# Kernel tuning notes

Hardware: AMD Instinct MI355X
Metric: run time of the kernel (lower is better)

The kernel has to match this reference:

```python
import jax, jax.numpy as jnp
import numpy as np

OFFSET_BINS = np.array([0.0, 0.00794435329, 0.0158887021, 0.0238330509, 0.0317773996,
                        0.0397217484, 0.0476660972, 0.0556104459, 0.0635547947,
                        0.0714991435, 0.08], dtype=np.float32)
BIN_WEIGHTS = jnp.array([0.16652107, 0.21488856, 0.37031708, 0.55618503, 0.75124664,
                         0.93943357, 1.07824539, 1.19423112, 1.55731375, 2.34173634],
                        dtype=jnp.float32)
RADIUS = 0.005
FAR = 1.0e5
EPS = 1e-7


def setup_inputs():
    key = jax.random.key(0)
    ks = jax.random.split(key, 10)
    B, N, M, C = 4, 2048, 4096, 5
    return {
        'pred_grasps': jax.random.normal(ks[0], (B, N, 4, 4), jnp.float32) * 0.1,
        'pred_scores': jax.random.uniform(ks[1], (B, N, 1), jnp.float32, 1e-4, 1.0 - 1e-4),
        'pred_points': jax.random.uniform(ks[2], (B, N, 3), jnp.float32) * 0.1,
        'grasp_width_head': jax.random.normal(ks[3], (B, 10, N), jnp.float32),
        'pos_contact_points': jax.random.uniform(ks[4], (B, M, 3), jnp.float32) * 0.1,
        'pos_contact_width': jax.random.uniform(ks[5], (B, M), jnp.float32) * 0.08,
        'pos_contact_rot': jax.random.normal(ks[6], (B, M, 3, 3), jnp.float32),
        'pos_contact_trans': jax.random.uniform(ks[7], (B, M, 3), jnp.float32) * 0.1,
        'gripper_control_points': jax.random.normal(ks[8], (1, C, 3), jnp.float32) * 0.05,
        'gripper_control_points_sym': jax.random.normal(ks[9], (1, C, 3), jnp.float32) * 0.05,
        'epoch': 0,
    }


def _gather(a, idx):
    # a: (B, M, ...), idx: (B, N) -> (B, N, ...)
    return jax.vmap(lambda x, j: x[j])(a, idx)


def _pairwise_sq(a, b):
    # a: (B,N,3), b: (B,M,3) -> (B,N,M) squared distances via norm expansion
    an = jnp.sum(a * a, -1)
    bn = jnp.sum(b * b, -1)
    cross = jnp.einsum('bnd,bmd->bnm', a, b)
    return jnp.maximum(an[:, :, None] + bn[:, None, :] - 2.0 * cross, 0.0)


def _pair_min_cp(P, G):
    # P,G: (B,N,C,3) control point sets -> (B,N) min_j sum_{c,d}(P_i - G_j)^2
    pn = jnp.sum(P * P, axis=(2, 3))
    gn = jnp.sum(G * G, axis=(2, 3))
    cross = jnp.einsum('bicd,bjcd->bij', P, G)  # (B,N,N)
    sq = pn[:, :, None] + gn[:, None, :] - 2.0 * cross
    return jnp.min(sq, axis=2)


def _forward(pred_grasps, pred_scores, pred_points, grasp_width_head,
             pos_contact_points, pos_contact_width, pos_contact_rot,
             pos_contact_trans, gripper_control_points, gripper_control_points_sym):
    B, N, _ = pred_points.shape
    # ---- labels: nearest GT contact per predicted point (nsample=1) ----
    d2 = _pairwise_sq(pred_points, pos_contact_points)          # (B,N,M)
    idx = jnp.argmin(d2, axis=2)                                 # (B,N)
    min_d2 = jnp.take_along_axis(d2, idx[:, :, None], axis=2)[..., 0]
    width_label = _gather(pos_contact_width, idx)[..., None]     # (B,N,1)
    success = (min_d2 < RADIUS ** 2).astype(jnp.float32)[..., None]  # (B,N,1)
    rot_label = _gather(pos_contact_rot, idx)                    # (B,N,3,3)
    trans_label = _gather(pos_contact_trans, idx)                # (B,N,3)

    pos_in_view = jnp.clip(jnp.sum(success, axis=1), 1.0, None)  # (B,1)

    # ---- binary score loss with balanced pos/neg sampling ----
    p = jnp.clip(pred_scores, EPS, 1.0 - EPS)
    bce = -(success * jnp.log(p) + (1.0 - success) * jnp.log(1.0 - p))[..., 0]  # (B,N)
    pos = success[..., 0]
    neg = 1.0 - pos
    n_pos = jnp.sum(pos, axis=1)                                 # (B,)
    r = jax.random.uniform(jax.random.key(42), (B, N))
    pri = jnp.where(neg > 0.5, r, jnp.inf)
    rank = jnp.argsort(jnp.argsort(pri, axis=1), axis=1)         # random ranks over negatives
    k = jnp.where(n_pos > 0, n_pos, 2.0)
    sel_neg = ((rank < k[:, None]) & (neg > 0.5)).astype(jnp.float32)
    sel = pos + sel_neg
    bin_ce_loss = jnp.mean(jnp.sum(bce * sel, axis=1) / jnp.maximum(jnp.sum(sel, axis=1), 1.0))

    # ---- width loss: multihot bins + weighted BCE-with-logits ----
    lo = jnp.asarray(OFFSET_BINS[:-1])
    hi = jnp.asarray(OFFSET_BINS[1:])
    multihot = ((width_label >= lo) & (width_label < hi)).astype(jnp.float32)  # (B,N,10)
    x = jnp.transpose(grasp_width_head, (0, 2, 1))               # (B,N,10)
    bcew = jnp.maximum(x, 0.0) - x * multihot + jnp.log1p(jnp.exp(-jnp.abs(x)))
    wl = jnp.mean(BIN_WEIGHTS[None, None, :] * bcew, axis=2)     # (B,N)
    width_loss = jnp.mean(jnp.sum(wl * pos, axis=1, keepdims=True) / pos_in_view)

    # ---- ADD-S loss ----
    mask = success > 0.5                                          # (B,N,1)
    rot_l = jnp.where(mask[..., None], rot_label, FAR)
    trans_l = jnp.where(mask, trans_label, FAR)
    cp = gripper_control_points[0]                                # (C,3)
    cps = gripper_control_points_sym[0]
    pred_rot = pred_grasps[:, :, :3, :3]
    pred_trans = pred_grasps[:, :, :3, 3]
    P = jnp.einsum('bnij,cj->bnci', pred_rot, cp) + pred_trans[:, :, None, :]
    G = jnp.einsum('bnij,cj->bnci', rot_l, cp) + trans_l[:, :, None, :]
    Gs = jnp.einsum('bnij,cj->bnci', rot_l, cps) + trans_l[:, :, None, :]
    m = jnp.minimum(_pair_min_cp(P, G), _pair_min_cp(P, Gs))     # (B,N)
    min_adds = pos * jnp.sqrt(jnp.maximum(m, 0.0) + 1e-12)
    adds = jnp.sum(pred_scores[..., 0] * min_adds, axis=1) / pos_in_view[:, 0]
    adds_loss = jnp.mean(adds)

    total_loss = bin_ce_loss + width_loss + 3.0 * adds_loss
    return total_loss, bin_ce_loss, width_loss, adds_loss


def reference(pred_grasps, pred_scores, pred_points, grasp_width_head,
              pos_contact_points, pos_contact_width, pos_contact_rot,
              pos_contact_trans, gripper_control_points, gripper_control_points_sym, epoch):
    return _forward(pred_grasps, pred_scores, pred_points, grasp_width_head,
                    pos_contact_points, pos_contact_width, pos_contact_rot,
                    pos_contact_trans, gripper_control_points, gripper_control_points_sym)
```

## Files before the change

kernel.cpp:

```cpp
#include <hip/hip_runtime.h>
#include <math.h>

#define B_ 4
#define N_ 2048
#define M_ 4096

#define ADDS_BLOCKS (B_ * (N_ / 16) * 2)
#define RANK_BLOCKS (B_ * (N_ / 16))

__constant__ float c_LO[10] = {0.0f, 0.00794435329f, 0.0158887021f, 0.0238330509f,
                               0.0317773996f, 0.0397217484f, 0.0476660972f,
                               0.0556104459f, 0.0635547947f, 0.0714991435f};
__constant__ float c_HI[10] = {0.00794435329f, 0.0158887021f, 0.0238330509f,
                               0.0317773996f, 0.0397217484f, 0.0476660972f,
                               0.0556104459f, 0.0635547947f, 0.0714991435f, 0.08f};
__constant__ float c_BW[10] = {0.16652107f, 0.21488856f, 0.37031708f, 0.55618503f,
                               0.75124664f, 0.93943357f, 1.07824539f, 1.19423112f,
                               1.55731375f, 2.34173634f};

#define R2_ 2.5e-05f
#define FAR_ 100000.0f
#define EPS_ 1e-07f

__device__ inline unsigned rotl32(unsigned x, int d) { return (x << d) | (x >> (32 - d)); }

__device__ inline void threefry2x32_42(unsigned x0, unsigned x1, unsigned& o0, unsigned& o1) {
    const unsigned k0 = 0u, k1 = 42u;
    const unsigned k2 = k0 ^ k1 ^ 0x1BD11BDAu;
    const unsigned ks[3] = {k0, k1, k2};
    const int rot[2][4] = {{13, 15, 26, 6}, {17, 29, 16, 24}};
    unsigned v0 = x0 + k0;
    unsigned v1 = x1 + k1;
#pragma unroll
    for (int i = 0; i < 5; ++i) {
        const int* r = rot[i & 1];
#pragma unroll
        for (int j = 0; j < 4; ++j) {
            v0 += v1;
            v1 = rotl32(v1, r[j]);
            v1 ^= v0;
        }
        v0 += ks[(i + 1) % 3];
        v1 += ks[(i + 2) % 3] + (unsigned)(i + 1);
    }
    o0 = v0; o1 = v1;
}

__device__ inline float bits_to_uniform(unsigned bits) {
    float f = __uint_as_float((bits >> 9) | 0x3f800000u) - 1.0f;
    return fmaxf(0.0f, f);
}

__device__ inline float jax_uniform_r(int flat) {
    unsigned o0, o1;
    if (flat < 4096) {
        threefry2x32_42((unsigned)flat, (unsigned)(flat + 4096), o0, o1);
        return bits_to_uniform(o0);
    } else {
        threefry2x32_42((unsigned)(flat - 4096), (unsigned)flat, o0, o1);
        return bits_to_uniform(o1);
    }
}

__global__ __launch_bounds__(256, 4) void nn_prep_kernel(
        const float* __restrict__ ppts, const float* __restrict__ pcp,
        const float* __restrict__ pred_grasps,
        const float* __restrict__ rot, const float* __restrict__ trans,
        const float* __restrict__ cp, const float* __restrict__ cps,
        int* __restrict__ idx_out, float* __restrict__ d2_out,
        float* __restrict__ Pout, float* __restrict__ Gt,
        int* __restrict__ counters) {
    if (blockIdx.x == 0 && threadIdx.x == 0) { counters[0] = 0; counters[1] = 0; }
    int blk = blockIdx.x;
    int b = blk / (N_ / 8);
    int tile = blk % (N_ / 8);
    int tid = threadIdx.x;
    int ig = tid & 1;
    int part = tid >> 1;
    int i0 = tile * 8 + ig * 4;

    float ax[4], ay[4], az[4], an[4];
#pragma unroll
    for (int ii = 0; ii < 4; ++ii) {
        const float* pp = ppts + ((size_t)b * N_ + i0 + ii) * 3;
        ax[ii] = pp[0]; ay[ii] = pp[1]; az[ii] = pp[2];
        an[ii] = ax[ii] * ax[ii] + ay[ii] * ay[ii] + az[ii] * az[ii];
    }

    const float4* pb4 = reinterpret_cast<const float4*>(pcp + (size_t)b * M_ * 3);
    float best[4] = {INFINITY, INFINITY, INFINITY, INFINITY};
    int bidx[4] = {0, 0, 0, 0};
    for (int g = 0; g < 8; ++g) {
        int grp = g * 128 + part;
        float4 q0 = pb4[grp * 3 + 0];
        float4 q1 = pb4[grp * 3 + 1];
        float4 q2 = pb4[grp * 3 + 2];
        float px[4] = {q0.x, q0.w, q1.z, q2.y};
        float py[4] = {q0.y, q1.x, q1.w, q2.z};
        float pz[4] = {q0.z, q1.y, q2.x, q2.w};
#pragma unroll
        for (int k = 0; k < 4; ++k) {
            float bn = px[k] * px[k] + py[k] * py[k] + pz[k] * pz[k];
            int j = grp * 4 + k;
#pragma unroll
            for (int ii = 0; ii < 4; ++ii) {
                float cross = ax[ii] * px[k] + ay[ii] * py[k] + az[ii] * pz[k];
                float d = an[ii] + bn - 2.0f * cross;
                d = fmaxf(d, 0.0f);
                if (d < best[ii]) { best[ii] = d; bidx[ii] = j; }
            }
        }
    }

    __shared__ float sd[8][128];
    __shared__ int si[8][128];
    __shared__ int win_bi[8];
    __shared__ float win_bb[8];
    __shared__ float rt[8][12];
#pragma unroll
    for (int ii = 0; ii < 4; ++ii) {
        sd[ig * 4 + ii][part] = best[ii];
        si[ig * 4 + ii][part] = bidx[ii];
    }
    __syncthreads();

    {
        int i2 = tid >> 5, r = tid & 31;
        float bb = sd[i2][r * 4];
        int bi = si[i2][r * 4];
#pragma unroll
        for (int p = 1; p < 4; ++p) {
            float dv = sd[i2][r * 4 + p];
            int iv = si[i2][r * 4 + p];
            if (dv < bb || (dv == bb && iv < bi)) { bb = dv; bi = iv; }
        }
        __syncthreads();
        sd[i2][r] = bb; si[i2][r] = bi;
    }
    __syncthreads();
    if (tid < 64) {
        int i2 = tid >> 3, r = tid & 7;
        float bb = sd[i2][r * 4];
        int bi = si[i2][r * 4];
#pragma unroll
        for (int p = 1; p < 4; ++p) {
            float dv = sd[i2][r * 4 + p];
            int iv = si[i2][r * 4 + p];
            if (dv < bb || (dv == bb && iv < bi)) { bb = dv; bi = iv; }
        }
        __syncthreads();
        sd[i2][r] = bb; si[i2][r] = bi;
    } else {
        __syncthreads();
    }
    __syncthreads();
    if (tid < 8) {
        float bb = sd[tid][0];
        int bi = si[tid][0];
#pragma unroll
        for (int p = 1; p < 8; ++p) {
            float dv = sd[tid][p];
            int iv = si[tid][p];
            if (dv < bb || (dv == bb && iv < bi)) { bb = dv; bi = iv; }
        }
        int n = tile * 8 + tid;
        idx_out[b * N_ + n] = bi;
        d2_out[b * N_ + n] = bb;
        win_bi[tid] = bi;
        win_bb[tid] = bb;
    }
    __syncthreads();

    if (tid < 96) {
        int n2 = tid / 12, c = tid % 12;
        int bi2 = win_bi[n2];
        bool succ2 = win_bb[n2] < R2_;
        float v;
        if (succ2) {
            v = (c < 9) ? rot[((size_t)b * M_ + bi2) * 9 + c]
                        : trans[((size_t)b * M_ + bi2) * 3 + (c - 9)];
        } else {
            v = FAR_;
        }
        rt[n2][c] = v;
    }
    __syncthreads();

    if (tid < 8) {
        int n = tile * 8 + tid;
        size_t i = (size_t)b * N_ + n;
        const float* g = pred_grasps + i * 16;
        float R[3][3] = {{g[0], g[1], g[2]}, {g[4], g[5], g[6]}, {g[8], g[9], g[10]}};
        float t[3] = {g[3], g[7], g[11]};

        float* P = Pout + i * 16;
        float pn = 0.0f;
#pragma unroll
        for (int c = 0; c < 5; ++c) {
            float cx = cp[c * 3], cy = cp[c * 3 + 1], cz = cp[c * 3 + 2];
#pragma unroll
            for (int kk = 0; kk < 3; ++kk) {
                float v = R[kk][0] * cx + R[kk][1] * cy + R[kk][2] * cz + t[kk];
                P[c * 3 + kk] = v;
                pn += v * v;
            }
        }
        P[15] = pn;

        float RL[3][3] = {{rt[tid][0], rt[tid][1], rt[tid][2]},
                          {rt[tid][3], rt[tid][4], rt[tid][5]},
                          {rt[tid][6], rt[tid][7], rt[tid][8]}};
        float TL[3] = {rt[tid][9], rt[tid][10], rt[tid][11]};

        float* gtb = Gt + ((size_t)b * 8 * N_ + n) * 4;
        float gn = 0.0f, gsn = 0.0f;
#pragma unroll
        for (int c = 0; c < 5; ++c) {
            float cx = cp[c * 3], cy = cp[c * 3 + 1], cz = cp[c * 3 + 2];
#pragma unroll
            for (int kk = 0; kk < 3; ++kk) {
                int comp = c * 3 + kk;
                float v = RL[kk][0] * cx + RL[kk][1] * cy + RL[kk][2] * cz + TL[kk];
                gtb[(size_t)(comp >> 2) * (N_ * 4) + (comp & 3)] = v;
                gn += v * v;
            }
        }
        gtb[(size_t)(15 >> 2) * (N_ * 4) + (15 & 3)] = gn;
#pragma unroll
        for (int c = 0; c < 5; ++c) {
            float cx = cps[c * 3], cy = cps[c * 3 + 1], cz = cps[c * 3 + 2];
#pragma unroll
            for (int kk = 0; kk < 3; ++kk) {
                int comp = 16 + c * 3 + kk;
                float v = RL[kk][0] * cx + RL[kk][1] * cy + RL[kk][2] * cz + TL[kk];
                gtb[(size_t)(comp >> 2) * (N_ * 4) + (comp & 3)] = v;
                gsn += v * v;
            }
        }
        gtb[(size_t)(31 >> 2) * (N_ * 4) + (31 & 3)] = gsn;
    }
}

__global__ __launch_bounds__(256, 4) void work_kernel(
        const float* __restrict__ Parr, const float4* __restrict__ Gt4,
        float* __restrict__ mOut2,
        const float* __restrict__ d2w, float* __restrict__ selws) {
    __shared__ __align__(16) char smem[9600];
    int bid = blockIdx.x;
    int tid = threadIdx.x;

    if (bid < ADDS_BLOCKS) {
        int b = bid / (2 * (N_ / 16));
        int rem = bid % (2 * (N_ / 16));
        int tile = rem >> 1;
        int jh = rem & 1;
        int w = tid >> 6;
        int lane = tid & 63;
        int i0 = tile * 16 + w * 4;

        const float4* P4 = reinterpret_cast<const float4*>(Parr) +
                           ((size_t)b * N_ + i0) * 4;
        float Pv[4][16];
#pragma unroll
        for (int h = 0; h < 4; ++h)
#pragma unroll
            for (int q = 0; q < 4; ++q) {
                float4 v = P4[h * 4 + q];
                Pv[h][q * 4 + 0] = v.x; Pv[h][q * 4 + 1] = v.y;
                Pv[h][q * 4 + 2] = v.z; Pv[h][q * 4 + 3] = v.w;
            }

        const float4* gq = Gt4 + (size_t)b * 8 * N_;
        float best[4] = {INFINITY, INFINITY, INFINITY, INFINITY};
        int jb0 = jh * (N_ / 128);
        for (int jb = jb0; jb < jb0 + (N_ / 128); ++jb) {
            int j = jb * 64 + lane;
            float g[16];
            {
                float4 h0 = gq[(size_t)0 * N_ + j];
                float4 h1 = gq[(size_t)1 * N_ + j];
                float4 h2 = gq[(size_t)2 * N_ + j];
                float4 h3 = gq[(size_t)3 * N_ + j];
                g[0] = h0.x; g[1] = h0.y; g[2] = h0.z; g[3] = h0.w;
                g[4] = h1.x; g[5] = h1.y; g[6] = h1.z; g[7] = h1.w;
                g[8] = h2.x; g[9] = h2.y; g[10] = h2.z; g[11] = h2.w;
                g[12] = h3.x; g[13] = h3.y; g[14] = h3.z; g[15] = h3.w;
            }
            float s1[4];
            {
                float d[4] = {0.0f, 0.0f, 0.0f, 0.0f};
#pragma unroll
                for (int q = 0; q < 15; ++q)
#pragma unroll
                    for (int ii = 0; ii < 4; ++ii) d[ii] += Pv[ii][q] * g[q];
#pragma unroll
                for (int ii = 0; ii < 4; ++ii) s1[ii] = Pv[ii][15] + g[15] - 2.0f * d[ii];
            }
            {
                float4 h0 = gq[(size_t)4 * N_ + j];
                float4 h1 = gq[(size_t)5 * N_ + j];
                float4 h2 = gq[(size_t)6 * N_ + j];
                float4 h3 = gq[(size_t)7 * N_ + j];
                g[0] = h0.x; g[1] = h0.y; g[2] = h0.z; g[3] = h0.w;
                g[4] = h1.x; g[5] = h1.y; g[6] = h1.z; g[7] = h1.w;
                g[8] = h2.x; g[9] = h2.y; g[10] = h2.z; g[11] = h2.w;
                g[12] = h3.x; g[13] = h3.y; g[14] = h3.z; g[15] = h3.w;
            }
            {
                float d[4] = {0.0f, 0.0f, 0.0f, 0.0f};
#pragma unroll
                for (int q = 0; q < 15; ++q)
#pragma unroll
                    for (int ii = 0; ii < 4; ++ii) d[ii] += Pv[ii][q] * g[q];
#pragma unroll
                for (int ii = 0; ii < 4; ++ii) {
                    float s2 = Pv[ii][15] + g[15] - 2.0f * d[ii];
                    best[ii] = fminf(best[ii], fminf(s1[ii], s2));
                }
            }
        }
#pragma unroll
        for (int m = 32; m > 0; m >>= 1) {
#pragma unroll
            for (int ii = 0; ii < 4; ++ii)
                best[ii] = fminf(best[ii], __shfl_xor(best[ii], m));
        }
        if (lane == 0) {
#pragma unroll
            for (int ii = 0; ii < 4; ++ii)
                mOut2[(size_t)(b * N_ + i0 + ii) * 2 + jh] = best[ii];
        }
    } else {
        int rid = bid - ADDS_BLOCKS;
        int b = rid / (N_ / 16);
        int tile = rid % (N_ / 16);
        int n_local = tid & 15;
        int part = tid >> 4;

        float* pri = (float*)smem;
        int* cnt_sh = (int*)(smem + 8192);
        __shared__ int s_npos;
        if (tid == 0) s_npos = 0;
        __syncthreads();

        int lp = 0;
        for (int q = tid; q < N_; q += 256) {
            bool pos = d2w[b * N_ + q] < R2_;
            pri[q] = pos ? INFINITY : jax_uniform_r(b * N_ + q);
            if (pos) lp++;
        }
        atomicAdd(&s_npos, lp);
        __syncthreads();

        int n = tile * 16 + n_local;
        float ra = pri[n];

        int cnt = 0;
        const float4* p4 = reinterpret_cast<const float4*>(pri);
        for (int o = 0; o < 8; ++o) {
            float4 v[4];
#pragma unroll
            for (int k = 0; k < 4; ++k) v[k] = p4[part + (o * 4 + k) * 16];
#pragma unroll
            for (int k = 0; k < 4; ++k) {
                int qb = (part + (o * 4 + k) * 16) * 4;
                cnt += ((v[k].x < ra) || (v[k].x == ra && (qb + 0) < n)) ? 1 : 0;
                cnt += ((v[k].y < ra) || (v[k].y == ra && (qb + 1) < n)) ? 1 : 0;
                cnt += ((v[k].z < ra) || (v[k].z == ra && (qb + 2) < n)) ? 1 : 0;
                cnt += ((v[k].w < ra) || (v[k].w == ra && (qb + 3) < n)) ? 1 : 0;
            }
        }
        cnt_sh[part * 17 + n_local] = cnt;
        __syncthreads();

        if (tid < 16) {
            int tot = 0;
#pragma unroll
            for (int p = 0; p < 16; ++p) tot += cnt_sh[p * 17 + tid];
            int npos = s_npos;
            int kk = (npos > 0) ? npos : 2;
            int n2 = tile * 16 + tid;
            float r2 = pri[n2];
            selws[b * N_ + n2] = (r2 == INFINITY) ? 1.0f : ((tot < kk) ? 1.0f : 0.0f);
        }
    }
}

__global__ __launch_bounds__(256) void finalize_kernel(
        const float* __restrict__ scores, const float* __restrict__ gwh,
        const float* __restrict__ pcw, const int* __restrict__ idxw,
        const float* __restrict__ d2w, const float* __restrict__ mw2,
        const float* __restrict__ selws,
        float* __restrict__ partials, int* __restrict__ counters,
        float* __restrict__ out) {
    int fid = blockIdx.x;
    int b = fid >> 3;
    int part = fid & 7;
    int tid = threadIdx.x;
    int n = part * 256 + tid;
    __shared__ float wsum[4][5];

    float sc = scores[b * N_ + n];
    float pcl = fminf(fmaxf(sc, EPS_), 0.9999999f);
    bool pos = d2w[b * N_ + n] < R2_;
    float s = pos ? 1.0f : 0.0f;
    float bce = -(s * logf(pcl) + (1.0f - s) * logf(1.0f - pcl));
    float selv = selws[b * N_ + n];
    float sum_sel = selv;
    float sum_bce = bce * selv;
    float sum_pos = s;
    float sum_wl = 0.0f, sum_adds = 0.0f;
    if (pos) {
        int jx = idxw[b * N_ + n];
        float w = pcw[b * M_ + jx];
        float acc = 0.0f;
#pragma unroll
        for (int jb = 0; jb < 10; ++jb) {
            float x = gwh[((size_t)b * 10 + jb) * N_ + n];
            float mh = (w >= c_LO[jb] && w < c_HI[jb]) ? 1.0f : 0.0f;
            float bw = fmaxf(x, 0.0f) - x * mh + log1pf(expf(-fabsf(x)));
            acc += c_BW[jb] * bw;
        }
        sum_wl = acc * 0.1f;
        float mv = fminf(mw2[(size_t)(b * N_ + n) * 2 + 0],
                         mw2[(size_t)(b * N_ + n) * 2 + 1]);
        sum_adds = sc * sqrtf(fmaxf(mv, 0.0f) + 1e-12f);
    }

    float v0 = sum_sel, v1 = sum_bce, v2 = sum_wl, v3 = sum_adds, v4 = sum_pos;
#pragma unroll
    for (int off = 32; off > 0; off >>= 1) {
        v0 += __shfl_down(v0, off);
        v1 += __shfl_down(v1, off);
        v2 += __shfl_down(v2, off);
        v3 += __shfl_down(v3, off);
        v4 += __shfl_down(v4, off);
    }
    int wv = tid >> 6, lane = tid & 63;
    if (lane == 0) {
        wsum[wv][0] = v0; wsum[wv][1] = v1; wsum[wv][2] = v2;
        wsum[wv][3] = v3; wsum[wv][4] = v4;
    }
    __syncthreads();
    if (tid == 0) {
        float t0 = 0, t1 = 0, t2 = 0, t3 = 0, t4 = 0;
#pragma unroll
        for (int w = 0; w < 4; ++w) {
            t0 += wsum[w][0]; t1 += wsum[w][1]; t2 += wsum[w][2];
            t3 += wsum[w][3]; t4 += wsum[w][4];
        }
        float* pp = partials + (size_t)fid * 5;
        pp[0] = t0; pp[1] = t1; pp[2] = t2; pp[3] = t3; pp[4] = t4;
        __threadfence();
        int old = atomicAdd(&counters[1], 1);
        if (old == 32 - 1) {
            __threadfence();
            float bin = 0, wid = 0, ad = 0;
#pragma unroll
            for (int b2 = 0; b2 < B_; ++b2) {
                float u0 = 0, u1 = 0, u2 = 0, u3 = 0, u4 = 0;
#pragma unroll
                for (int p2 = 0; p2 < 8; ++p2) {
                    const float* q = partials + (size_t)(b2 * 8 + p2) * 5;
                    u0 += q[0]; u1 += q[1]; u2 += q[2]; u3 += q[3]; u4 += q[4];
                }
                float piv = fmaxf(u4, 1.0f);
                bin += u1 / fmaxf(u0, 1.0f);
                wid += u2 / piv;
                ad  += u3 / piv;
            }
            bin *= 0.25f; wid *= 0.25f; ad *= 0.25f;
            out[0] = bin + wid + 3.0f * ad;
            out[1] = bin;
            out[2] = wid;
            out[3] = ad;
        }
    }
}

extern "C" void kernel_launch(void* const* d_in, const int* in_sizes, int n_in,
                              void* d_out, int out_size, void* d_ws, size_t ws_size,
                              hipStream_t stream) {
    const float* pred_grasps = (const float*)d_in[0];
    const float* pred_scores = (const float*)d_in[1];
    const float* pred_points = (const float*)d_in[2];
    const float* gwh         = (const float*)d_in[3];
    const float* pcp         = (const float*)d_in[4];
    const float* pcw         = (const float*)d_in[5];
    const float* pcr         = (const float*)d_in[6];
    const float* pct         = (const float*)d_in[7];
    const float* cp          = (const float*)d_in[8];
    const float* cps         = (const float*)d_in[9];
    (void)in_sizes; (void)n_in; (void)out_size; (void)ws_size;

    float* ws = (float*)d_ws;
    int*   idxw  = (int*)ws;
    float* d2w   = ws + 8192;
    float* Pw    = ws + 16384;
    float* Gt    = Pw + 131072;
    float* mw2   = Gt + 262144;
    float* selws = mw2 + 16384;
    float* parts = selws + 8192;
    int*   ctrs  = (int*)(parts + 160);
    float* outp  = (float*)d_out;

    hipLaunchKernelGGL(nn_prep_kernel, dim3(B_ * (N_ / 8)), dim3(256), 0, stream,
                       pred_points, pcp, pred_grasps, pcr, pct, cp, cps,
                       idxw, d2w, Pw, Gt, ctrs);
    hipLaunchKernelGGL(work_kernel, dim3(ADDS_BLOCKS + RANK_BLOCKS), dim3(256), 0, stream,
                       Pw, (const float4*)Gt, mw2, d2w, selws);
    hipLaunchKernelGGL(finalize_kernel, dim3(B_ * 8), dim3(256), 0, stream,
                       pred_scores, gwh, pcw, idxw, d2w, mw2, selws, parts, ctrs, outp);
}
```

Before: 132.2 us.

## Fuse finalize into work kernel using atomic completion counter and spin-wait

Merges the finalize kernel into the work kernel as its last 32 blocks. Each producer block bumps a release atomic counter when done, and the finalize blocks spin on it with s_sleep before reducing. This removes one kernel launch and the launch gap between the two stages. The spin-wait relies on the producer blocks being scheduled before or alongside the waiting blocks, and waiting blocks hold CU slots while they spin.

```diff
diff --git a/kernel.cpp b/kernel.cpp
--- a/kernel.cpp
+++ b/kernel.cpp
@@ -7,6 +7,8 @@
 
 #define ADDS_BLOCKS (B_ * (N_ / 16) * 2)
 #define RANK_BLOCKS (B_ * (N_ / 16))
+#define PROD_BLOCKS (ADDS_BLOCKS + RANK_BLOCKS)
+#define FIN_BLOCKS (B_ * 8)
 
 __constant__ float c_LO[10] = {0.0f, 0.00794435329f, 0.0158887021f, 0.0238330509f,
                                0.0317773996f, 0.0397217484f, 0.0476660972f,
@@ -241,10 +243,14 @@
     }
 }
 
-__global__ __launch_bounds__(256, 4) void work_kernel(
+__global__ __launch_bounds__(256, 4) void mega_kernel(
         const float* __restrict__ Parr, const float4* __restrict__ Gt4,
         float* __restrict__ mOut2,
-        const float* __restrict__ d2w, float* __restrict__ selws) {
+        const float* __restrict__ d2w, float* __restrict__ selws,
+        const float* __restrict__ scores, const float* __restrict__ gwh,
+        const float* __restrict__ pcw, const int* __restrict__ idxw,
+        float* __restrict__ partials, int* __restrict__ counters,
+        float* __restrict__ out) {
     __shared__ __align__(16) char smem[9600];
     int bid = blockIdx.x;
     int tid = threadIdx.x;
@@ -330,7 +336,13 @@
             for (int ii = 0; ii < 4; ++ii)
                 mOut2[(size_t)(b * N_ + i0 + ii) * 2 + jh] = best[ii];
         }
-    } else {
+        __syncthreads();
+        if (tid == 0) {
+            __threadfence();
+            __hip_atomic_fetch_add(&counters[0], 1, __ATOMIC_RELEASE,
+                                   __HIP_MEMORY_SCOPE_AGENT);
+        }
+    } else if (bid < PROD_BLOCKS) {
         int rid = bid - ADDS_BLOCKS;
         int b = rid / (N_ / 16);
         int tile = rid % (N_ / 16);
@@ -383,97 +395,104 @@
             float r2 = pri[n2];
             selws[b * N_ + n2] = (r2 == INFINITY) ? 1.0f : ((tot < kk) ? 1.0f : 0.0f);
         }
-    }
-}
-
-__global__ __launch_bounds__(256) void finalize_kernel(
-        const float* __restrict__ scores, const float* __restrict__ gwh,
-        const float* __restrict__ pcw, const int* __restrict__ idxw,
-        const float* __restrict__ d2w, const float* __restrict__ mw2,
-        const float* __restrict__ selws,
-        float* __restrict__ partials, int* __restrict__ counters,
-        float* __restrict__ out) {
-    int fid = blockIdx.x;
-    int b = fid >> 3;
-    int part = fid & 7;
-    int tid = threadIdx.x;
-    int n = part * 256 + tid;
-    __shared__ float wsum[4][5];
-
-    float sc = scores[b * N_ + n];
-    float pcl = fminf(fmaxf(sc, EPS_), 0.9999999f);
-    bool pos = d2w[b * N_ + n] < R2_;
-    float s = pos ? 1.0f : 0.0f;
-    float bce = -(s * logf(pcl) + (1.0f - s) * logf(1.0f - pcl));
-    float selv = selws[b * N_ + n];
-    float sum_sel = selv;
-    float sum_bce = bce * selv;
-    float sum_pos = s;
-    float sum_wl = 0.0f, sum_adds = 0.0f;
-    if (pos) {
-        int jx = idxw[b * N_ + n];
-        float w = pcw[b * M_ + jx];
-        float acc = 0.0f;
-#pragma unroll
-        for (int jb = 0; jb < 10; ++jb) {
-            float x = gwh[((size_t)b * 10 + jb) * N_ + n];
-            float mh = (w >= c_LO[jb] && w < c_HI[jb]) ? 1.0f : 0.0f;
-            float bw = fmaxf(x, 0.0f) - x * mh + log1pf(expf(-fabsf(x)));
-            acc += c_BW[jb] * bw;
-        }
-        sum_wl = acc * 0.1f;
-        float mv = fminf(mw2[(size_t)(b * N_ + n) * 2 + 0],
-                         mw2[(size_t)(b * N_ + n) * 2 + 1]);
-        sum_adds = sc * sqrtf(fmaxf(mv, 0.0f) + 1e-12f);
-    }
-
-    float v0 = sum_sel, v1 = sum_bce, v2 = sum_wl, v3 = sum_adds, v4 = sum_pos;
-#pragma unroll
-    for (int off = 32; off > 0; off >>= 1) {
-        v0 += __shfl_down(v0, off);
-        v1 += __shfl_down(v1, off);
-        v2 += __shfl_down(v2, off);
-        v3 += __shfl_down(v3, off);
-        v4 += __shfl_down(v4, off);
-    }
-    int wv = tid >> 6, lane = tid & 63;
-    if (lane == 0) {
-        wsum[wv][0] = v0; wsum[wv][1] = v1; wsum[wv][2] = v2;
-        wsum[wv][3] = v3; wsum[wv][4] = v4;
-    }
-    __syncthreads();
-    if (tid == 0) {
-        float t0 = 0, t1 = 0, t2 = 0, t3 = 0, t4 = 0;
-#pragma unroll
-        for (int w = 0; w < 4; ++w) {
-            t0 += wsum[w][0]; t1 += wsum[w][1]; t2 += wsum[w][2];
-            t3 += wsum[w][3]; t4 += wsum[w][4];
-        }
-        float* pp = partials + (size_t)fid * 5;
-        pp[0] = t0; pp[1] = t1; pp[2] = t2; pp[3] = t3; pp[4] = t4;
+        __syncthreads();
+        if (tid == 0) {
+            __threadfence();
+            __hip_atomic_fetch_add(&counters[0], 1, __ATOMIC_RELEASE,
+                                   __HIP_MEMORY_SCOPE_AGENT);
+        }
+    } else {
+        int fid = bid - PROD_BLOCKS;
+        int b = fid >> 3;
+        int part = fid & 7;
+        int n = part * 256 + tid;
+        float* wsum = (float*)smem;
+
+        if (tid == 0) {
+            while (__hip_atomic_load(&counters[0], __ATOMIC_ACQUIRE,
+                                     __HIP_MEMORY_SCOPE_AGENT) < PROD_BLOCKS) {
+                __builtin_amdgcn_s_sleep(2);
+            }
+        }
+        __syncthreads();
         __threadfence();
-        int old = atomicAdd(&counters[1], 1);
-        if (old == 32 - 1) {
+
+        float sc = scores[b * N_ + n];
+        float pcl = fminf(fmaxf(sc, EPS_), 0.9999999f);
+        bool pos = d2w[b * N_ + n] < R2_;
+        float s = pos ? 1.0f : 0.0f;
+        float bce = -(s * logf(pcl) + (1.0f - s) * logf(1.0f - pcl));
+        float selv = selws[b * N_ + n];
+        float sum_sel = selv;
+        float sum_bce = bce * selv;
+        float sum_pos = s;
+        float sum_wl = 0.0f, sum_adds = 0.0f;
+        if (pos) {
+            int jx = idxw[b * N_ + n];
+            float w = pcw[b * M_ + jx];
+            float acc = 0.0f;
+#pragma unroll
+            for (int jb = 0; jb < 10; ++jb) {
+                float x = gwh[((size_t)b * 10 + jb) * N_ + n];
+                float mh = (w >= c_LO[jb] && w < c_HI[jb]) ? 1.0f : 0.0f;
+                float bw = fmaxf(x, 0.0f) - x * mh + log1pf(expf(-fabsf(x)));
+                acc += c_BW[jb] * bw;
+            }
+            sum_wl = acc * 0.1f;
+            float mv = fminf(mOut2[(size_t)(b * N_ + n) * 2 + 0],
+                             mOut2[(size_t)(b * N_ + n) * 2 + 1]);
+            sum_adds = sc * sqrtf(fmaxf(mv, 0.0f) + 1e-12f);
+        }
+
+        float v0 = sum_sel, v1 = sum_bce, v2 = sum_wl, v3 = sum_adds, v4 = sum_pos;
+#pragma unroll
+        for (int off = 32; off > 0; off >>= 1) {
+            v0 += __shfl_down(v0, off);
+            v1 += __shfl_down(v1, off);
+            v2 += __shfl_down(v2, off);
+            v3 += __shfl_down(v3, off);
+            v4 += __shfl_down(v4, off);
+        }
+        int wv = tid >> 6, lane = tid & 63;
+        if (lane == 0) {
+            wsum[wv * 5 + 0] = v0; wsum[wv * 5 + 1] = v1; wsum[wv * 5 + 2] = v2;
+            wsum[wv * 5 + 3] = v3; wsum[wv * 5 + 4] = v4;
+        }
+        __syncthreads();
+        if (tid == 0) {
+            float t0 = 0, t1 = 0, t2 = 0, t3 = 0, t4 = 0;
+#pragma unroll
+            for (int w = 0; w < 4; ++w) {
+                t0 += wsum[w * 5 + 0]; t1 += wsum[w * 5 + 1]; t2 += wsum[w * 5 + 2];
+                t3 += wsum[w * 5 + 3]; t4 += wsum[w * 5 + 4];
+            }
+            float* pp = partials + (size_t)fid * 5;
+            pp[0] = t0; pp[1] = t1; pp[2] = t2; pp[3] = t3; pp[4] = t4;
             __threadfence();
-            float bin = 0, wid = 0, ad = 0;
-#pragma unroll
-            for (int b2 = 0; b2 < B_; ++b2) {
-                float u0 = 0, u1 = 0, u2 = 0, u3 = 0, u4 = 0;
-#pragma unroll
-                for (int p2 = 0; p2 < 8; ++p2) {
-                    const float* q = partials + (size_t)(b2 * 8 + p2) * 5;
-                    u0 += q[0]; u1 += q[1]; u2 += q[2]; u3 += q[3]; u4 += q[4];
+            int old = __hip_atomic_fetch_add(&counters[1], 1, __ATOMIC_ACQ_REL,
+                                             __HIP_MEMORY_SCOPE_AGENT);
+            if (old == FIN_BLOCKS - 1) {
+                __threadfence();
+                float bin = 0, wid = 0, ad = 0;
+#pragma unroll
+                for (int b2 = 0; b2 < B_; ++b2) {
+                    float u0 = 0, u1 = 0, u2 = 0, u3 = 0, u4 = 0;
+#pragma unroll
+                    for (int p2 = 0; p2 < 8; ++p2) {
+                        const float* q = partials + (size_t)(b2 * 8 + p2) * 5;
+                        u0 += q[0]; u1 += q[1]; u2 += q[2]; u3 += q[3]; u4 += q[4];
+                    }
+                    float piv = fmaxf(u4, 1.0f);
+                    bin += u1 / fmaxf(u0, 1.0f);
+                    wid += u2 / piv;
+                    ad  += u3 / piv;
                 }
-                float piv = fmaxf(u4, 1.0f);
-                bin += u1 / fmaxf(u0, 1.0f);
-                wid += u2 / piv;
-                ad  += u3 / piv;
-            }
-            bin *= 0.25f; wid *= 0.25f; ad *= 0.25f;
-            out[0] = bin + wid + 3.0f * ad;
-            out[1] = bin;
-            out[2] = wid;
-            out[3] = ad;
+                bin *= 0.25f; wid *= 0.25f; ad *= 0.25f;
+                out[0] = bin + wid + 3.0f * ad;
+                out[1] = bin;
+                out[2] = wid;
+                out[3] = ad;
+            }
         }
     }
 }
@@ -507,8 +526,7 @@
     hipLaunchKernelGGL(nn_prep_kernel, dim3(B_ * (N_ / 8)), dim3(256), 0, stream,
                        pred_points, pcp, pred_grasps, pcr, pct, cp, cps,
                        idxw, d2w, Pw, Gt, ctrs);
-    hipLaunchKernelGGL(work_kernel, dim3(ADDS_BLOCKS + RANK_BLOCKS), dim3(256), 0, stream,
-                       Pw, (const float4*)Gt, mw2, d2w, selws);
-    hipLaunchKernelGGL(finalize_kernel, dim3(B_ * 8), dim3(256), 0, stream,
-                       pred_scores, gwh, pcw, idxw, d2w, mw2, selws, parts, ctrs, outp);
+    hipLaunchKernelGGL(mega_kernel, dim3(PROD_BLOCKS + FIN_BLOCKS), dim3(256), 0, stream,
+                       Pw, (const float4*)Gt, mw2, d2w, selws,
+                       pred_scores, gwh, pcw, idxw, parts, ctrs, outp);
 }
```

After: 194.0 us. 46.7% more time.
